# Kernel optimization log

Hardware: AMD Instinct MI355X
Metric: run time of the kernel (lower is better)

Reference implementation:

```python
import jax, jax.numpy as jnp
import numpy as np

DIM = 1024
NUM_HEADS = 16
HEAD_DIM = DIM // NUM_HEADS
BINDING_BIAS = 0.5
SCALE = HEAD_DIM ** -0.5


def setup_inputs() -> dict:
    key = jax.random.key(0)
    ks = jax.random.split(key, 10)
    B, S, D = 2, 2048, DIM
    std = D ** -0.5
    return {
        "x": jax.random.normal(ks[0], (B, S, D), jnp.float32),
        "binding_matrix": jax.random.uniform(ks[1], (S, S), jnp.float32),
        "Wq": jax.random.normal(ks[2], (D, D), jnp.float32) * std,
        "bq": jnp.zeros((D,), jnp.float32),
        "Wk": jax.random.normal(ks[3], (D, D), jnp.float32) * std,
        "bk": jnp.zeros((D,), jnp.float32),
        "Wv": jax.random.normal(ks[4], (D, D), jnp.float32) * std,
        "bv": jnp.zeros((D,), jnp.float32),
        "Wo": jax.random.normal(ks[5], (D, D), jnp.float32) * std,
        "bo": jnp.zeros((D,), jnp.float32),
    }


def reference(x, binding_matrix, Wq, bq, Wk, bk, Wv, bv, Wo, bo):
    B, S, D = x.shape
    H, Hd = NUM_HEADS, HEAD_DIM
    # projections -> [B, H, S, Hd]
    q = (x @ Wq + bq).reshape(B, S, H, Hd).transpose(0, 2, 1, 3)
    k = (x @ Wk + bk).reshape(B, S, H, Hd).transpose(0, 2, 1, 3)
    v = (x @ Wv + bv).reshape(B, S, H, Hd).transpose(0, 2, 1, 3)
    # scores [B, H, S, S] with additive binding bias
    attn = jnp.einsum("bhqd,bhkd->bhqk", q, k) * SCALE
    attn = attn + BINDING_BIAS * binding_matrix[None, None, :, :]
    attn = jax.nn.softmax(attn, axis=-1)
    out = jnp.einsum("bhqk,bhkd->bhqd", attn, v)
    out = out.transpose(0, 2, 1, 3).reshape(B, S, D)
    return out @ Wo + bo
```

## Files before the change

### kernel.cpp

```cpp
#include <hip/hip_runtime.h>

#define DEV static __device__ __forceinline__

typedef __attribute__((ext_vector_type(4))) float f32x4;
typedef __attribute__((ext_vector_type(8))) __bf16 bfv8;
typedef __attribute__((ext_vector_type(8))) short s8v;
typedef __attribute__((ext_vector_type(4))) short s4v;

DEV short f2bf(float f) {
    unsigned u = __float_as_uint(f);
    u = (u + 0x7fffu + ((u >> 16) & 1u)) >> 16;
    return (short)u;
}
DEV float bf2f(short s) { return __uint_as_float(((unsigned)(unsigned short)s) << 16); }

DEV void gload16(const void* g, void* l) {
    __builtin_amdgcn_global_load_lds(
        (const __attribute__((address_space(1))) void*)g,
        (__attribute__((address_space(3))) void*)l, 16, 0, 0);
}

DEV f32x4 mfma16(bfv8 a, bfv8 b, f32x4 c) {
    return __builtin_amdgcn_mfma_f32_16x16x32_bf16(a, b, c, 0, 0, 0);
}

DEV float max3f(float a, float b, float c) {
    float d;
    asm("v_max3_f32 %0, %1, %2, %3" : "=v"(d) : "v"(a), "v"(b), "v"(c));
    return d;
}
DEV unsigned cvtpk(float lo, float hi) {
    unsigned w;
    asm("v_cvt_pk_bf16_f32 %0, %1, %2" : "=v"(w) : "v"(lo), "v"(hi));
    return w;
}

DEV bfv8 ldsfrag(const short* base, int row, int slog) {
    int sp = slog ^ (row & 7);
    return *reinterpret_cast<const bfv8*>(base + row * 64 + sp * 8);
}

__global__ void k_cvt(const float* __restrict__ in, short* __restrict__ out, float s) {
    int i = blockIdx.x * blockDim.x + threadIdx.x;
    const float4* p = (const float4*)in + (size_t)i * 2;
    float4 a = p[0], b = p[1];
    s8v o;
    o[0] = f2bf(a.x * s); o[1] = f2bf(a.y * s); o[2] = f2bf(a.z * s); o[3] = f2bf(a.w * s);
    o[4] = f2bf(b.x * s); o[5] = f2bf(b.y * s); o[6] = f2bf(b.z * s); o[7] = f2bf(b.w * s);
    reinterpret_cast<s8v*>(out)[i] = o;
}

__global__ void k_transpose4(
    const float* __restrict__ W0, const float* __restrict__ W1,
    const float* __restrict__ W2, const float* __restrict__ W3,
    short* __restrict__ T0, short* __restrict__ T1,
    short* __restrict__ T2, short* __restrict__ T3, float s0)
{
    __shared__ float tl[32][33];
    const int z = blockIdx.z;
    const float* W = z == 0 ? W0 : z == 1 ? W1 : z == 2 ? W2 : W3;
    short* Wt = z == 0 ? T0 : z == 1 ? T1 : z == 2 ? T2 : T3;
    const float s = z == 0 ? s0 : 1.f;
    int tx = threadIdx.x & 31, ty = threadIdx.x >> 5;
    int nb = blockIdx.x * 32, kb = blockIdx.y * 32;
#pragma unroll
    for (int i = 0; i < 4; i++)
        tl[ty + i * 8][tx] = W[(kb + ty + i * 8) * 1024 + nb + tx];
    __syncthreads();
#pragma unroll
    for (int i = 0; i < 4; i++)
        Wt[(nb + ty + i * 8) * 1024 + kb + tx] = f2bf(tl[tx][ty + i * 8] * s);
}

template <int EPI>
DEV void gemm_body(const short* __restrict__ A, const short* __restrict__ Bt,
                   const float* __restrict__ bias, void* __restrict__ outp,
                   float bscale, int row0, int col0, short* As, short* Bs)
{
    const int t = threadIdx.x, lane = t & 63;
    const int wv = t >> 6, wr = wv >> 1, wc = wv & 1;
    const int g = lane >> 4, c = lane & 15;

    const f32x4 z4 = {0.f, 0.f, 0.f, 0.f};
    f32x4 acc[2][4];
#pragma unroll
    for (int m = 0; m < 2; m++)
#pragma unroll
        for (int n = 0; n < 4; n++) acc[m][n] = z4;

    for (int kt = 0; kt < 16; ++kt) {
        const int k0 = kt * 64;
        const short* Ag = A + row0 * 1024 + k0;
        const short* Bg = Bt + col0 * 1024 + k0;
#pragma unroll
        for (int j = 0; j < 2; j++) {
            int idx = j * 256 + t;
            int row = idx >> 3, sp = idx & 7, sl = sp ^ (row & 7);
            gload16(Ag + row * 1024 + sl * 8, As + idx * 8);
        }
#pragma unroll
        for (int j = 0; j < 4; j++) {
            int idx = j * 256 + t;
            int row = idx >> 3, sp = idx & 7, sl = sp ^ (row & 7);
            gload16(Bg + row * 1024 + sl * 8, Bs + idx * 8);
        }
        __syncthreads();

        bfv8 af[2][2], bfr[4][2];
#pragma unroll
        for (int m = 0; m < 2; m++)
#pragma unroll
            for (int ks = 0; ks < 2; ks++)
                af[m][ks] = ldsfrag(As, wr * 32 + m * 16 + c, ks * 4 + g);
#pragma unroll
        for (int n = 0; n < 4; n++)
#pragma unroll
            for (int ks = 0; ks < 2; ks++)
                bfr[n][ks] = ldsfrag(Bs, wc * 64 + n * 16 + c, ks * 4 + g);
        __builtin_amdgcn_s_setprio(1);
#pragma unroll
        for (int m = 0; m < 2; m++)
#pragma unroll
            for (int n = 0; n < 4; n++)
#pragma unroll
                for (int ks = 0; ks < 2; ks++)
                    acc[m][n] = mfma16(af[m][ks], bfr[n][ks], acc[m][n]);
        __builtin_amdgcn_s_setprio(0);
        __syncthreads();
    }

#pragma unroll
    for (int n = 0; n < 4; n++) {
        const int gc = col0 + wc * 64 + n * 16 + c;
        const float bvl = bias[gc] * bscale;
        const int h = gc >> 6, d = gc & 63;
#pragma unroll
        for (int m = 0; m < 2; m++) {
            const int gr = row0 + wr * 32 + m * 16 + g * 4;
            if (EPI == 2) {
                float* O = (float*)outp;
#pragma unroll
                for (int r = 0; r < 4; r++) O[(gr + r) * 1024 + gc] = acc[m][n][r] + bvl;
            } else {
                const int b = gr >> 11, sr = gr & 2047;
                short* O = (short*)outp;
                if (EPI == 0) {
                    int base = ((b * 16 + h) * 2048 + sr) * 64 + d;
#pragma unroll
                    for (int r = 0; r < 4; r++) O[base + r * 64] = f2bf(acc[m][n][r] + bvl);
                } else {
                    s4v vv;
#pragma unroll
                    for (int r = 0; r < 4; r++) vv[r] = f2bf(acc[m][n][r] + bvl);
                    const int s6 = sr & 63;
                    const int qp = (sr & ~63) | (s6 & 35) | ((s6 & 12) << 1) | ((s6 & 16) >> 2);
                    *reinterpret_cast<s4v*>(O + ((b * 16 + h) * 64 + d) * 2048 + qp) = vv;
                }
            }
        }
    }
}

__global__ __launch_bounds__(256, 2) void k_gemm3(
    const short* __restrict__ A,
    const short* __restrict__ WqT, const short* __restrict__ WkT, const short* __restrict__ WvT,
    const float* __restrict__ bq, const float* __restrict__ bk, const float* __restrict__ bv,
    short* __restrict__ Qs, short* __restrict__ Kst, short* __restrict__ Vts, float scq)
{
    __shared__ alignas(16) short As[64 * 64];
    __shared__ alignas(16) short Bs[128 * 64];
    const int which = blockIdx.y >> 3;
    const int col0 = (blockIdx.y & 7) * 128;
    const int row0 = blockIdx.x * 64;
    if (which == 0)
        gemm_body<0>(A, WqT, bq, Qs, scq, row0, col0, As, Bs);
    else if (which == 1)
        gemm_body<0>(A, WkT, bk, Kst, 1.f, row0, col0, As, Bs);
    else
        gemm_body<1>(A, WvT, bv, Vts, 1.f, row0, col0, As, Bs);
}

__global__ __launch_bounds__(256, 2) void k_gemmO(
    const short* __restrict__ A, const short* __restrict__ Bt,
    const float* __restrict__ bias, float* __restrict__ outp)
{
    __shared__ alignas(16) short As[64 * 64];
    __shared__ alignas(16) short Bs[128 * 64];
    gemm_body<2>(A, Bt, bias, outp, 1.f, blockIdx.x * 64, blockIdx.y * 128, As, Bs);
}

__global__ __launch_bounds__(256, 5) void k_attn(
    const short* __restrict__ Q, const short* __restrict__ K,
    const short* __restrict__ Vt, const short* __restrict__ bb,
    short* __restrict__ Ob)
{
    __shared__ alignas(16) short Ks[2][64 * 64];
    __shared__ alignas(16) short Vs[2][64 * 64];
    const int t = threadIdx.x, lane = t & 63;
    const int wv = t >> 6, g = lane >> 4, c = lane & 15;
    const int qt = blockIdx.x, bh = blockIdx.y;
    const int b = bh >> 4, h = bh & 15;
    const short* Qb = Q + bh * 2048 * 64;
    const short* Kb = K + bh * 2048 * 64;
    const short* Vb = Vt + bh * 64 * 2048;
    const int q0 = qt * 64 + wv * 16;

    bfv8 qf[2];
#pragma unroll
    for (int ks = 0; ks < 2; ks++)
        qf[ks] = *reinterpret_cast<const bfv8*>(Qb + (q0 + c) * 64 + ks * 32 + g * 8);

    const f32x4 z4 = {0.f, 0.f, 0.f, 0.f};
    f32x4 oa[4];
#pragma unroll
    for (int nd = 0; nd < 4; nd++) oa[nd] = z4;
    f32x4 lacc = z4;
    float mrun = 20.0f;

    s8v ob_;
#pragma unroll
    for (int i = 0; i < 8; i++) ob_[i] = (short)0x3F80;
    const bfv8 ones = __builtin_bit_cast(bfv8, ob_);

    const int idx0 = t, idx1 = 256 + t;
    const int r0 = idx0 >> 3, s0 = ((idx0 & 7) ^ (r0 & 7)) * 8;
    const int r1 = idx1 >> 3, s1 = ((idx1 & 7) ^ (r1 & 7)) * 8;
    const short* kp0 = Kb + r0 * 64 + s0;
    const short* kp1 = Kb + r1 * 64 + s1;
    const short* vp0 = Vb + r0 * 2048 + s0;
    const short* vp1 = Vb + r1 * 2048 + s1;
    const short* bbp = bb + (size_t)(q0 + c) * 2048 + 4 * g;

    const int cx = c & 7;
    const int fofs0 = c * 128 + ((g ^ cx) << 4);
    const int fofs1 = c * 128 + (((4 + g) ^ cx) << 4);

    gload16(kp0, &Ks[0][idx0 * 8]);
    gload16(kp1, &Ks[0][idx1 * 8]);
    gload16(vp0, &Vs[0][idx0 * 8]);
    gload16(vp1, &Vs[0][idx1 * 8]);
    kp0 += 4096; kp1 += 4096; vp0 += 64; vp1 += 64;
    s4v bn[4];
#pragma unroll
    for (int n = 0; n < 4; n++) bn[n] = *reinterpret_cast<const s4v*>(bbp + n * 16);
    bbp += 64;
    __syncthreads();

    for (int kt = 0; kt < 32; ++kt) {
        const int cur = kt & 1;
        f32x4 cb[4];
#pragma unroll
        for (int n = 0; n < 4; n++)
#pragma unroll
            for (int r = 0; r < 4; r++) cb[n][r] = bf2f(bn[n][r]);
        if (kt < 31) {
            const int nb = cur ^ 1;
            gload16(kp0, &Ks[nb][idx0 * 8]);
            gload16(kp1, &Ks[nb][idx1 * 8]);
            gload16(vp0, &Vs[nb][idx0 * 8]);
            gload16(vp1, &Vs[nb][idx1 * 8]);
            kp0 += 4096; kp1 += 4096; vp0 += 64; vp1 += 64;
#pragma unroll
            for (int n = 0; n < 4; n++) bn[n] = *reinterpret_cast<const s4v*>(bbp + n * 16);
            bbp += 64;
        }

        const char* Kc = (const char*)&Ks[cur][0];
        const char* Vc = (const char*)&Vs[cur][0];

        f32x4 sc[4];
        __builtin_amdgcn_s_setprio(1);
#pragma unroll
        for (int n = 0; n < 4; n++) {
            bfv8 k0 = *reinterpret_cast<const bfv8*>(Kc + fofs0 + n * 2048);
            bfv8 k1 = *reinterpret_cast<const bfv8*>(Kc + fofs1 + n * 2048);
            sc[n] = mfma16(k0, qf[0], cb[n]);
            sc[n] = mfma16(k1, qf[1], sc[n]);
        }
        __builtin_amdgcn_s_setprio(0);

#pragma unroll
        for (int n = 0; n < 4; n++)
#pragma unroll
            for (int r = 0; r < 4; r++)
                sc[n][r] = __builtin_amdgcn_exp2f(sc[n][r] - mrun);

        unsigned w0[4], w1[4];
#pragma unroll
        for (int n = 0; n < 4; n++) {
            w0[n] = cvtpk(sc[n][0], sc[n][1]);
            w1[n] = cvtpk(sc[n][2], sc[n][3]);
        }
        typedef struct { unsigned a, b, c2, d; } u4;
        u4 q0w; q0w.a = w0[0]; q0w.b = w1[0]; q0w.c2 = w0[1]; q0w.d = w1[1];
        u4 q1w; q1w.a = w0[2]; q1w.b = w1[2]; q1w.c2 = w0[3]; q1w.d = w1[3];
        const bfv8 pf0 = __builtin_bit_cast(bfv8, q0w);
        const bfv8 pf1 = __builtin_bit_cast(bfv8, q1w);

        __builtin_amdgcn_s_setprio(1);
#pragma unroll
        for (int nd = 0; nd < 4; nd++) {
            bfv8 v0 = *reinterpret_cast<const bfv8*>(Vc + fofs0 + nd * 2048);
            bfv8 v1 = *reinterpret_cast<const bfv8*>(Vc + fofs1 + nd * 2048);
            oa[nd] = mfma16(v0, pf0, oa[nd]);
            oa[nd] = mfma16(v1, pf1, oa[nd]);
        }
        lacc = mfma16(ones, pf0, lacc);
        lacc = mfma16(ones, pf1, lacc);
        __builtin_amdgcn_s_setprio(0);

        float t0 = fmaxf(max3f(sc[0][0], sc[0][1], sc[0][2]), sc[0][3]);
        float t1 = fmaxf(max3f(sc[1][0], sc[1][1], sc[1][2]), sc[1][3]);
        float t2 = fmaxf(max3f(sc[2][0], sc[2][1], sc[2][2]), sc[2][3]);
        float t3 = fmaxf(max3f(sc[3][0], sc[3][1], sc[3][2]), sc[3][3]);
        float pemax = fmaxf(max3f(t0, t1, t2), t3);
        if (!__all(pemax <= 2896.0f)) {
            float rmax = fmaxf(pemax, __shfl_xor(pemax, 16));
            rmax = fmaxf(rmax, __shfl_xor(rmax, 32));
            if (rmax > 2896.0f) {
                const float corr = 1.0f / rmax;
                mrun += __log2f(rmax);
#pragma unroll
                for (int nd = 0; nd < 4; nd++)
#pragma unroll
                    for (int r = 0; r < 4; r++) oa[nd][r] *= corr;
#pragma unroll
                for (int r = 0; r < 4; r++) lacc[r] *= corr;
            }
        }
        __syncthreads();
    }

    const float rl = 1.0f / lacc[0];
    const size_t srow = (size_t)(b * 2048 + q0 + c);
#pragma unroll
    for (int nd = 0; nd < 4; nd++) {
        s4v st;
#pragma unroll
        for (int r = 0; r < 4; r++) st[r] = f2bf(oa[nd][r] * rl);
        *reinterpret_cast<s4v*>(Ob + srow * 1024 + h * 64 + nd * 16 + 4 * g) = st;
    }
}

extern "C" void kernel_launch(void* const* d_in, const int* in_sizes, int n_in,
                              void* d_out, int out_size, void* d_ws, size_t ws_size,
                              hipStream_t stream)
{
    (void)in_sizes; (void)n_in; (void)out_size; (void)ws_size;
    const float* x    = (const float*)d_in[0];
    const float* bind = (const float*)d_in[1];
    const float* Wq   = (const float*)d_in[2];
    const float* bq   = (const float*)d_in[3];
    const float* Wk   = (const float*)d_in[4];
    const float* bk   = (const float*)d_in[5];
    const float* Wv   = (const float*)d_in[6];
    const float* bv   = (const float*)d_in[7];
    const float* Wo   = (const float*)d_in[8];
    const float* bo   = (const float*)d_in[9];

    char* ws = (char*)d_ws;
    const size_t MB = (size_t)1 << 20;
    short* xb   = (short*)(ws + 0 * MB);
    short* Wqt  = (short*)(ws + 8 * MB);
    short* Wkt  = (short*)(ws + 10 * MB);
    short* Wvt  = (short*)(ws + 12 * MB);
    short* Wot  = (short*)(ws + 14 * MB);
    short* bbm  = (short*)(ws + 16 * MB);
    short* Qs   = (short*)(ws + 24 * MB);
    short* Kst  = (short*)(ws + 32 * MB);
    short* Vts  = (short*)(ws + 40 * MB);
    short* Obuf = (short*)(ws + 48 * MB);

    const float LOG2E = 1.4426950408889634f;
    const float SCQ = 0.125f * LOG2E;
    const float SCB = 0.5f * LOG2E;

    k_cvt<<<2048, 256, 0, stream>>>(x, xb, 1.f);
    k_cvt<<<2048, 256, 0, stream>>>(bind, bbm, SCB);
    k_transpose4<<<dim3(32, 32, 4), 256, 0, stream>>>(Wq, Wk, Wv, Wo,
                                                      Wqt, Wkt, Wvt, Wot, SCQ);
    k_gemm3<<<dim3(64, 24), 256, 0, stream>>>(xb, Wqt, Wkt, Wvt, bq, bk, bv,
                                              Qs, Kst, Vts, SCQ);
    k_attn<<<dim3(32, 32), 256, 0, stream>>>(Qs, Kst, Vts, bbm, Obuf);
    k_gemmO<<<dim3(64, 8), 256, 0, stream>>>(Obuf, Wot, bo, (float*)d_out);
}
```

Baseline: 150.3 us.

## Software-pipeline attention loop: defer PV MFMA one tile behind QK and softmax

Restructures the attention inner loop so the P·V MFMAs for tile kt-1 run before the QK^T MFMAs and exp for tile kt. This lets the matrix unit overlap with the exponentials and max reduction. V gets a triple-buffered LDS ring because the deferred tile must stay resident while the next one streams in. When a rescale happens, the pending probabilities are rescaled too. The cost is more LDS and registers, so launch bounds drop from 5 to 4 blocks per CU, reducing occupancy.

```diff
diff --git a/kernel.cpp b/kernel.cpp
--- a/kernel.cpp
+++ b/kernel.cpp
@@ -189,13 +189,13 @@
     gemm_body<2>(A, Bt, bias, outp, 1.f, blockIdx.x * 64, blockIdx.y * 128, As, Bs);
 }
 
-__global__ __launch_bounds__(256, 5) void k_attn(
+__global__ __launch_bounds__(256, 4) void k_attn(
     const short* __restrict__ Q, const short* __restrict__ K,
     const short* __restrict__ Vt, const short* __restrict__ bb,
     short* __restrict__ Ob)
 {
     __shared__ alignas(16) short Ks[2][64 * 64];
-    __shared__ alignas(16) short Vs[2][64 * 64];
+    __shared__ alignas(16) short Vs[3][64 * 64];
     const int t = threadIdx.x, lane = t & 63;
     const int wv = t >> 6, g = lane >> 4, c = lane & 15;
     const int qt = blockIdx.x, bh = blockIdx.y;
@@ -240,34 +240,49 @@
     gload16(vp0, &Vs[0][idx0 * 8]);
     gload16(vp1, &Vs[0][idx1 * 8]);
     kp0 += 4096; kp1 += 4096; vp0 += 64; vp1 += 64;
-    s4v bn[4];
-#pragma unroll
-    for (int n = 0; n < 4; n++) bn[n] = *reinterpret_cast<const s4v*>(bbp + n * 16);
+    s4v bnC[4], bnN[4];
+#pragma unroll
+    for (int n = 0; n < 4; n++) bnC[n] = *reinterpret_cast<const s4v*>(bbp + n * 16);
     bbp += 64;
     __syncthreads();
 
+    bfv8 pfA = {}, pfB = {};
+    int vwi = 1;
+
     for (int kt = 0; kt < 32; ++kt) {
-        const int cur = kt & 1;
         f32x4 cb[4];
 #pragma unroll
         for (int n = 0; n < 4; n++)
 #pragma unroll
-            for (int r = 0; r < 4; r++) cb[n][r] = bf2f(bn[n][r]);
+            for (int r = 0; r < 4; r++) cb[n][r] = bf2f(bnC[n][r]);
         if (kt < 31) {
-            const int nb = cur ^ 1;
-            gload16(kp0, &Ks[nb][idx0 * 8]);
-            gload16(kp1, &Ks[nb][idx1 * 8]);
-            gload16(vp0, &Vs[nb][idx0 * 8]);
-            gload16(vp1, &Vs[nb][idx1 * 8]);
+            gload16(kp0, &Ks[(kt + 1) & 1][idx0 * 8]);
+            gload16(kp1, &Ks[(kt + 1) & 1][idx1 * 8]);
+            gload16(vp0, &Vs[vwi][idx0 * 8]);
+            gload16(vp1, &Vs[vwi][idx1 * 8]);
             kp0 += 4096; kp1 += 4096; vp0 += 64; vp1 += 64;
 #pragma unroll
-            for (int n = 0; n < 4; n++) bn[n] = *reinterpret_cast<const s4v*>(bbp + n * 16);
+            for (int n = 0; n < 4; n++) bnN[n] = *reinterpret_cast<const s4v*>(bbp + n * 16);
             bbp += 64;
         }
-
-        const char* Kc = (const char*)&Ks[cur][0];
-        const char* Vc = (const char*)&Vs[cur][0];
-
+        vwi = (vwi == 2) ? 0 : vwi + 1;
+
+        if (kt > 0) {
+            const char* Vc = (const char*)&Vs[(kt - 1) % 3][0];
+            __builtin_amdgcn_s_setprio(1);
+#pragma unroll
+            for (int nd = 0; nd < 4; nd++) {
+                bfv8 v0 = *reinterpret_cast<const bfv8*>(Vc + fofs0 + nd * 2048);
+                bfv8 v1 = *reinterpret_cast<const bfv8*>(Vc + fofs1 + nd * 2048);
+                oa[nd] = mfma16(v0, pfA, oa[nd]);
+                oa[nd] = mfma16(v1, pfB, oa[nd]);
+            }
+            lacc = mfma16(ones, pfA, lacc);
+            lacc = mfma16(ones, pfB, lacc);
+            __builtin_amdgcn_s_setprio(0);
+        }
+
+        const char* Kc = (const char*)&Ks[kt & 1][0];
         f32x4 sc[4];
         __builtin_amdgcn_s_setprio(1);
 #pragma unroll
@@ -284,30 +299,6 @@
 #pragma unroll
             for (int r = 0; r < 4; r++)
                 sc[n][r] = __builtin_amdgcn_exp2f(sc[n][r] - mrun);
-
-        unsigned w0[4], w1[4];
-#pragma unroll
-        for (int n = 0; n < 4; n++) {
-            w0[n] = cvtpk(sc[n][0], sc[n][1]);
-            w1[n] = cvtpk(sc[n][2], sc[n][3]);
-        }
-        typedef struct { unsigned a, b, c2, d; } u4;
-        u4 q0w; q0w.a = w0[0]; q0w.b = w1[0]; q0w.c2 = w0[1]; q0w.d = w1[1];
-        u4 q1w; q1w.a = w0[2]; q1w.b = w1[2]; q1w.c2 = w0[3]; q1w.d = w1[3];
-        const bfv8 pf0 = __builtin_bit_cast(bfv8, q0w);
-        const bfv8 pf1 = __builtin_bit_cast(bfv8, q1w);
-
-        __builtin_amdgcn_s_setprio(1);
-#pragma unroll
-        for (int nd = 0; nd < 4; nd++) {
-            bfv8 v0 = *reinterpret_cast<const bfv8*>(Vc + fofs0 + nd * 2048);
-            bfv8 v1 = *reinterpret_cast<const bfv8*>(Vc + fofs1 + nd * 2048);
-            oa[nd] = mfma16(v0, pf0, oa[nd]);
-            oa[nd] = mfma16(v1, pf1, oa[nd]);
-        }
-        lacc = mfma16(ones, pf0, lacc);
-        lacc = mfma16(ones, pf1, lacc);
-        __builtin_amdgcn_s_setprio(0);
 
         float t0 = fmaxf(max3f(sc[0][0], sc[0][1], sc[0][2]), sc[0][3]);
         float t1 = fmaxf(max3f(sc[1][0], sc[1][1], sc[1][2]), sc[1][3]);
@@ -321,6 +312,10 @@
                 const float corr = 1.0f / rmax;
                 mrun += __log2f(rmax);
 #pragma unroll
+                for (int n = 0; n < 4; n++)
+#pragma unroll
+                    for (int r = 0; r < 4; r++) sc[n][r] *= corr;
+#pragma unroll
                 for (int nd = 0; nd < 4; nd++)
 #pragma unroll
                     for (int r = 0; r < 4; r++) oa[nd][r] *= corr;
@@ -328,7 +323,36 @@
                 for (int r = 0; r < 4; r++) lacc[r] *= corr;
             }
         }
+
+        {
+            unsigned w0[4], w1[4];
+#pragma unroll
+            for (int n = 0; n < 4; n++) {
+                w0[n] = cvtpk(sc[n][0], sc[n][1]);
+                w1[n] = cvtpk(sc[n][2], sc[n][3]);
+            }
+            typedef struct { unsigned a, b, c2, d; } u4;
+            u4 q0w; q0w.a = w0[0]; q0w.b = w1[0]; q0w.c2 = w0[1]; q0w.d = w1[1];
+            u4 q1w; q1w.a = w0[2]; q1w.b = w1[2]; q1w.c2 = w0[3]; q1w.d = w1[3];
+            pfA = __builtin_bit_cast(bfv8, q0w);
+            pfB = __builtin_bit_cast(bfv8, q1w);
+        }
+#pragma unroll
+        for (int n = 0; n < 4; n++) bnC[n] = bnN[n];
         __syncthreads();
+    }
+
+    {
+        const char* Vc = (const char*)&Vs[31 % 3][0];
+#pragma unroll
+        for (int nd = 0; nd < 4; nd++) {
+            bfv8 v0 = *reinterpret_cast<const bfv8*>(Vc + fofs0 + nd * 2048);
+            bfv8 v1 = *reinterpret_cast<const bfv8*>(Vc + fofs1 + nd * 2048);
+            oa[nd] = mfma16(v0, pfA, oa[nd]);
+            oa[nd] = mfma16(v1, pfB, oa[nd]);
+        }
+        lacc = mfma16(ones, pfA, lacc);
+        lacc = mfma16(ones, pfB, lacc);
     }
 
     const float rl = 1.0f / lacc[0];
```

Result: no change. 150.1 us (-0.1%).

## Double attention query tile per block and retile binding bias for coalesced loads

Applied to the files above, without the earlier changes.

The attention kernel now runs 512 threads (8 waves) per block, covering 128 query rows instead of 64. Each staged K/V tile is therefore reused by twice as many waves, and each thread issues one K and one V load instead of two. The binding-bias conversion kernel now writes a layout tiled by 16-column key chunks, so a wave's per-iteration bias reads hit contiguous memory rather than 2048-element row strides. The trade-off is half as many blocks and a changed occupancy bound (launch bounds 512,2), which may affect latency hiding.

```diff
diff --git a/kernel.cpp b/kernel.cpp
--- a/kernel.cpp
+++ b/kernel.cpp
@@ -48,6 +48,20 @@
     o[0] = f2bf(a.x * s); o[1] = f2bf(a.y * s); o[2] = f2bf(a.z * s); o[3] = f2bf(a.w * s);
     o[4] = f2bf(b.x * s); o[5] = f2bf(b.y * s); o[6] = f2bf(b.z * s); o[7] = f2bf(b.w * s);
     reinterpret_cast<s8v*>(out)[i] = o;
+}
+
+__global__ void k_cvtb(const float* __restrict__ in, short* __restrict__ out, float s) {
+    int i = blockIdx.x * blockDim.x + threadIdx.x;
+    int ktn = i >> 11, q = i & 2047;
+    const float4* p = reinterpret_cast<const float4*>(in + (size_t)q * 2048 + ktn * 16);
+    float4 a = p[0], b = p[1], cc = p[2], d = p[3];
+    s8v o0, o1;
+    o0[0] = f2bf(a.x * s); o0[1] = f2bf(a.y * s); o0[2] = f2bf(a.z * s); o0[3] = f2bf(a.w * s);
+    o0[4] = f2bf(b.x * s); o0[5] = f2bf(b.y * s); o0[6] = f2bf(b.z * s); o0[7] = f2bf(b.w * s);
+    o1[0] = f2bf(cc.x * s); o1[1] = f2bf(cc.y * s); o1[2] = f2bf(cc.z * s); o1[3] = f2bf(cc.w * s);
+    o1[4] = f2bf(d.x * s); o1[5] = f2bf(d.y * s); o1[6] = f2bf(d.z * s); o1[7] = f2bf(d.w * s);
+    s8v* dst = reinterpret_cast<s8v*>(out + (size_t)i * 16);
+    dst[0] = o0; dst[1] = o1;
 }
 
 __global__ void k_transpose4(
@@ -189,9 +203,9 @@
     gemm_body<2>(A, Bt, bias, outp, 1.f, blockIdx.x * 64, blockIdx.y * 128, As, Bs);
 }
 
-__global__ __launch_bounds__(256, 5) void k_attn(
+__global__ __launch_bounds__(512, 2) void k_attn(
     const short* __restrict__ Q, const short* __restrict__ K,
-    const short* __restrict__ Vt, const short* __restrict__ bb,
+    const short* __restrict__ Vt, const short* __restrict__ bbt,
     short* __restrict__ Ob)
 {
     __shared__ alignas(16) short Ks[2][64 * 64];
@@ -203,7 +217,7 @@
     const short* Qb = Q + bh * 2048 * 64;
     const short* Kb = K + bh * 2048 * 64;
     const short* Vb = Vt + bh * 64 * 2048;
-    const int q0 = qt * 64 + wv * 16;
+    const int q0 = qt * 128 + wv * 16;
 
     bfv8 qf[2];
 #pragma unroll
@@ -222,28 +236,24 @@
     for (int i = 0; i < 8; i++) ob_[i] = (short)0x3F80;
     const bfv8 ones = __builtin_bit_cast(bfv8, ob_);
 
-    const int idx0 = t, idx1 = 256 + t;
-    const int r0 = idx0 >> 3, s0 = ((idx0 & 7) ^ (r0 & 7)) * 8;
-    const int r1 = idx1 >> 3, s1 = ((idx1 & 7) ^ (r1 & 7)) * 8;
+    const int r0 = t >> 3, s0 = ((t & 7) ^ (r0 & 7)) * 8;
     const short* kp0 = Kb + r0 * 64 + s0;
-    const short* kp1 = Kb + r1 * 64 + s1;
     const short* vp0 = Vb + r0 * 2048 + s0;
-    const short* vp1 = Vb + r1 * 2048 + s1;
-    const short* bbp = bb + (size_t)(q0 + c) * 2048 + 4 * g;
+    const int dst8 = t * 8;
+    const short* bbp = bbt + (size_t)(q0 + c) * 16 + 4 * g;
 
     const int cx = c & 7;
     const int fofs0 = c * 128 + ((g ^ cx) << 4);
     const int fofs1 = c * 128 + (((4 + g) ^ cx) << 4);
 
-    gload16(kp0, &Ks[0][idx0 * 8]);
-    gload16(kp1, &Ks[0][idx1 * 8]);
-    gload16(vp0, &Vs[0][idx0 * 8]);
-    gload16(vp1, &Vs[0][idx1 * 8]);
-    kp0 += 4096; kp1 += 4096; vp0 += 64; vp1 += 64;
+    gload16(kp0, &Ks[0][dst8]);
+    gload16(vp0, &Vs[0][dst8]);
+    kp0 += 4096; vp0 += 64;
     s4v bn[4];
 #pragma unroll
-    for (int n = 0; n < 4; n++) bn[n] = *reinterpret_cast<const s4v*>(bbp + n * 16);
-    bbp += 64;
+    for (int n = 0; n < 4; n++)
+        bn[n] = *reinterpret_cast<const s4v*>(bbp + n * 32768);
+    bbp += 131072;
     __syncthreads();
 
     for (int kt = 0; kt < 32; ++kt) {
@@ -255,14 +265,13 @@
             for (int r = 0; r < 4; r++) cb[n][r] = bf2f(bn[n][r]);
         if (kt < 31) {
             const int nb = cur ^ 1;
-            gload16(kp0, &Ks[nb][idx0 * 8]);
-            gload16(kp1, &Ks[nb][idx1 * 8]);
-            gload16(vp0, &Vs[nb][idx0 * 8]);
-            gload16(vp1, &Vs[nb][idx1 * 8]);
-            kp0 += 4096; kp1 += 4096; vp0 += 64; vp1 += 64;
-#pragma unroll
-            for (int n = 0; n < 4; n++) bn[n] = *reinterpret_cast<const s4v*>(bbp + n * 16);
-            bbp += 64;
+            gload16(kp0, &Ks[nb][dst8]);
+            gload16(vp0, &Vs[nb][dst8]);
+            kp0 += 4096; vp0 += 64;
+#pragma unroll
+            for (int n = 0; n < 4; n++)
+                bn[n] = *reinterpret_cast<const s4v*>(bbp + n * 32768);
+            bbp += 131072;
         }
 
         const char* Kc = (const char*)&Ks[cur][0];
@@ -376,11 +385,11 @@
     const float SCB = 0.5f * LOG2E;
 
     k_cvt<<<2048, 256, 0, stream>>>(x, xb, 1.f);
-    k_cvt<<<2048, 256, 0, stream>>>(bind, bbm, SCB);
+    k_cvtb<<<1024, 256, 0, stream>>>(bind, bbm, SCB);
     k_transpose4<<<dim3(32, 32, 4), 256, 0, stream>>>(Wq, Wk, Wv, Wo,
                                                       Wqt, Wkt, Wvt, Wot, SCQ);
     k_gemm3<<<dim3(64, 24), 256, 0, stream>>>(xb, Wqt, Wkt, Wvt, bq, bk, bv,
                                               Qs, Kst, Vts, SCQ);
-    k_attn<<<dim3(32, 32), 256, 0, stream>>>(Qs, Kst, Vts, bbm, Obuf);
+    k_attn<<<dim3(16, 32), 512, 0, stream>>>(Qs, Kst, Vts, bbm, Obuf);
     k_gemmO<<<dim3(64, 8), 256, 0, stream>>>(Obuf, Wot, bo, (float*)d_out);
 }
```

New measurement: 125.4 us. 1.2x faster.
